# Kernel optimization log

Hardware: AMD Instinct MI355X
Metric: run time of the kernel (lower is better)

The kernel has to match this reference:

```python
import jax, jax.numpy as jnp
import numpy as np

LN_EPS = 1e-5


def _graph_conv(x, src, dst, W, b):
    # x: [N, D]; src, dst: [E]. Edge (src->dst): node n aggregates mean of
    # x[src] over edges whose dst == n (matches batch_edges[0][batch_edges[1]==n]).
    N = x.shape[0]
    agg_sum = jax.ops.segment_sum(x[src], dst, num_segments=N)            # [N, D]
    cnt = jax.ops.segment_sum(jnp.ones_like(src, dtype=x.dtype), dst, num_segments=N)
    agg = agg_sum / jnp.maximum(cnt, 1.0)[:, None]                        # zeros if no neighbors
    combined = jnp.concatenate([x, agg], axis=-1)                         # [N, 2D]
    return combined @ W + b


def _layer_norm(x, g, b):
    mu = jnp.mean(x, axis=-1, keepdims=True)
    var = jnp.var(x, axis=-1, keepdims=True)
    return (x - mu) * jax.lax.rsqrt(var + LN_EPS) * g + b


def setup_inputs() -> dict:
    key = jax.random.key(0)
    ks = jax.random.split(key, 16)
    B, N, E = 16, 10000, 160000
    IN, H, OUT, L = 19, 64, 32, 3
    s = lambda k, fan_in, shape: jax.random.normal(k, shape, jnp.float32) * (1.0 / np.sqrt(fan_in))
    return {
        "node_features": jax.random.normal(ks[0], (B, N, IN), jnp.float32),
        "edge_indices": jax.random.randint(ks[1], (B, 2, E), 0, N, jnp.int64),
        "batch_size": B,
        "enc_w1": s(ks[2], IN, (IN, H)), "enc_b1": jnp.zeros((H,), jnp.float32),
        "enc_w2": s(ks[3], H, (H, H)), "enc_b2": jnp.zeros((H,), jnp.float32),
        "conv_w": s(ks[4], 2 * H, (L, 2 * H, H)), "conv_b": jnp.zeros((L, H), jnp.float32),
        "ln_g": jnp.ones((L, H), jnp.float32), "ln_b": jnp.zeros((L, H), jnp.float32),
        "out_w": s(ks[5], H, (H, OUT)), "out_b": jnp.zeros((OUT,), jnp.float32),
    }


def reference(node_features, edge_indices, batch_size, enc_w1, enc_b1, enc_w2, enc_b2,
              conv_w, conv_b, ln_g, ln_b, out_w, out_b):
    # node encoder: Linear -> ReLU -> Linear
    x = jax.nn.relu(node_features @ enc_w1 + enc_b1) @ enc_w2 + enc_b2    # [B, N, H]
    src = edge_indices[:, 0, :]
    dst = edge_indices[:, 1, :]
    num_layers = conv_w.shape[0]
    conv = jax.vmap(_graph_conv, in_axes=(0, 0, 0, None, None))
    for i in range(num_layers):
        residual = x
        x = conv(x, src, dst, conv_w[i], conv_b[i])
        x = _layer_norm(x + residual, ln_g[i], ln_b[i])
        x = jax.nn.relu(x)
    return x @ out_w + out_b                                              # [B, N, 32]
```

## Files before the change

kernel.cpp:

```cpp
#include <hip/hip_runtime.h>
#include <hip/hip_fp16.h>

#define NB   16
#define NN   10000
#define NE   160000
#define NODES (NB*NN)
#define IN_F 19
#define HF   64
#define OUTF 32
#define LN_EPS 1e-5f
#define RANGE 625
#define NCHUNK 32
#define CHSZ (NE/NCHUNK)
#define BCAP 16384


__device__ inline unsigned pk_f16(float a, float b) {
    __half2 h = __float22half2_rn(float2{a, b});
    return *(unsigned*)&h;
}
__device__ inline float2 upk_f16(unsigned u) {
    __half2 h = *(__half2*)&u;
    return __half22float2(h);
}

__global__ __launch_bounds__(256) void enc1_kernel(
    const float* __restrict__ nf,
    const float* __restrict__ w1, const float* __restrict__ b1,
    __half* __restrict__ xh)
{
    int node = blockIdx.x * 256 + threadIdx.x;
    const float* p = nf + (size_t)node * IN_F;
    float a[IN_F];
#pragma unroll
    for (int k = 0; k < IN_F; ++k) a[k] = p[k];

    float h[HF];
#pragma unroll
    for (int j = 0; j < HF; ++j) h[j] = b1[j];
#pragma unroll
    for (int k = 0; k < IN_F; ++k) {
        float ak = a[k];
        const float* wr = w1 + k * HF;
#pragma unroll
        for (int j = 0; j < HF; ++j) h[j] = fmaf(ak, wr[j], h[j]);
    }

    uint4* dst = (uint4*)(xh + (size_t)node * HF);
#pragma unroll
    for (int q = 0; q < 8; ++q) {
        uint4 u;
        u.x = pk_f16(fmaxf(h[8*q+0],0.f), fmaxf(h[8*q+1],0.f));
        u.y = pk_f16(fmaxf(h[8*q+2],0.f), fmaxf(h[8*q+3],0.f));
        u.z = pk_f16(fmaxf(h[8*q+4],0.f), fmaxf(h[8*q+5],0.f));
        u.w = pk_f16(fmaxf(h[8*q+6],0.f), fmaxf(h[8*q+7],0.f));
        dst[q] = u;
    }
}

__global__ __launch_bounds__(256) void gemm64_kernel(
    __half* __restrict__ xh, const float* __restrict__ W, const float* __restrict__ bias)
{
    int lane = threadIdx.x & 63;
    int waveid = threadIdx.x >> 6;
    int half = __builtin_amdgcn_readfirstlane(waveid & 1);
    int nib = (waveid >> 1) * 64 + lane;
    int node = blockIdx.x * 128 + nib;
    const uint4* rp = (const uint4*)(xh + (size_t)node * HF);

    float acc[32];
    const float* b2 = bias + half * 32;
#pragma unroll
    for (int j = 0; j < 32; ++j) acc[j] = b2[j];

#pragma unroll 1
    for (int kc = 0; kc < HF; kc += 16) {
        uint4 u0 = rp[kc >> 3];
        uint4 u1 = rp[(kc >> 3) + 1];
        float av[16];
        float2 f;
        f = upk_f16(u0.x); av[0]=f.x;  av[1]=f.y;
        f = upk_f16(u0.y); av[2]=f.x;  av[3]=f.y;
        f = upk_f16(u0.z); av[4]=f.x;  av[5]=f.y;
        f = upk_f16(u0.w); av[6]=f.x;  av[7]=f.y;
        f = upk_f16(u1.x); av[8]=f.x;  av[9]=f.y;
        f = upk_f16(u1.y); av[10]=f.x; av[11]=f.y;
        f = upk_f16(u1.z); av[12]=f.x; av[13]=f.y;
        f = upk_f16(u1.w); av[14]=f.x; av[15]=f.y;
#pragma unroll
        for (int u = 0; u < 16; ++u) {
            const float* wr = W + (kc + u) * HF + half * 32;
#pragma unroll
            for (int j = 0; j < 32; ++j) acc[j] = fmaf(av[u], wr[j], acc[j]);
        }
    }

    __syncthreads();

    uint4* hdst = (uint4*)(xh + (size_t)node * HF + half * 32);
#pragma unroll
    for (int q = 0; q < 4; ++q) {
        uint4 u;
        u.x = pk_f16(acc[8*q+0], acc[8*q+1]);
        u.y = pk_f16(acc[8*q+2], acc[8*q+3]);
        u.z = pk_f16(acc[8*q+4], acc[8*q+5]);
        u.w = pk_f16(acc[8*q+6], acc[8*q+7]);
        hdst[q] = u;
    }
}

__global__ __launch_bounds__(256) void bucket_kernel(const int* __restrict__ ei,
                                                     int* __restrict__ gcur,
                                                     unsigned* __restrict__ bkt)
{
    __shared__ int lcnt[16];
    __shared__ int lcur[16];
    __shared__ int gbase[16];
    int b = blockIdx.x >> 5;
    int chunk = blockIdx.x & 31;
    int t = threadIdx.x;
    if (t < 16) { lcnt[t] = 0; lcur[t] = 0; }
    __syncthreads();

    const int* srcp = ei + (size_t)b * 2 * NE + chunk * CHSZ;
    const int* dstp = srcp + NE;

    for (int e = t; e < CHSZ; e += 256)
        atomicAdd(&lcnt[(unsigned)dstp[e] / RANGE], 1);
    __syncthreads();
    if (t < 16) gbase[t] = atomicAdd(&gcur[b * 16 + t], lcnt[t]);
    __syncthreads();

    for (int e = t; e < CHSZ; e += 256) {
        int d = dstp[e];
        int s = srcp[e];
        int j = (unsigned)d / RANGE;
        int ld = d - j * RANGE;
        int pos = gbase[j] + atomicAdd(&lcur[j], 1);
        if (pos < BCAP)
            bkt[(size_t)(b * 16 + j) * BCAP + pos] = (unsigned)s | ((unsigned)ld << 16);
    }
}

__global__ __launch_bounds__(512) void count2_kernel(const unsigned* __restrict__ bkt,
                                                     const int* __restrict__ gcur,
                                                     int* __restrict__ cnt)
{
    __shared__ int lcnt[RANGE];
    int bid = blockIdx.x;
    int b = bid >> 4, j = bid & 15;
    int t = threadIdx.x;
    for (int i = t; i < RANGE; i += 512) lcnt[i] = 0;
    __syncthreads();
    int n = min(gcur[bid], BCAP);
    const unsigned* bp = bkt + (size_t)bid * BCAP;
    for (int e = t; e < n; e += 512) atomicAdd(&lcnt[bp[e] >> 16], 1);
    __syncthreads();
    int base = b * NN + j * RANGE;
    for (int i = t; i < RANGE; i += 512) cnt[base + i] = lcnt[i];
}

__global__ __launch_bounds__(256) void scan_kernel(const int* __restrict__ cnt, int* __restrict__ off)
{
    __shared__ int sdata[256];
    int b = blockIdx.x, t = threadIdx.x;
    const int CH = 40;
    int lo = t * CH, hi = min(lo + CH, NN);
    int s = 0;
    for (int i = lo; i < hi; ++i) s += cnt[b * NN + i];
    sdata[t] = s;
    __syncthreads();
    for (int ofs = 1; ofs < 256; ofs <<= 1) {
        int v = (t >= ofs) ? sdata[t - ofs] : 0;
        __syncthreads();
        sdata[t] += v;
        __syncthreads();
    }
    int run = (t > 0) ? sdata[t - 1] : 0;
    for (int i = lo; i < hi; ++i) { off[b * NN + i] = run; run += cnt[b * NN + i]; }
}

__global__ __launch_bounds__(512) void fill2_kernel(const unsigned* __restrict__ bkt,
                                                    const int* __restrict__ gcur,
                                                    const int* __restrict__ off,
                                                    int* __restrict__ csr)
{
    __shared__ int lcur[RANGE];
    int bid = blockIdx.x;
    int b = bid >> 4, j = bid & 15;
    int t = threadIdx.x;
    for (int i = t; i < RANGE; i += 512) lcur[i] = 0;
    __syncthreads();
    int n = min(gcur[bid], BCAP);
    const unsigned* bp = bkt + (size_t)bid * BCAP;
    const int* offb = off + b * NN + j * RANGE;
    int* csrb = csr + (size_t)b * NE;
    for (int e = t; e < n; e += 512) {
        unsigned u = bp[e];
        int ld = u >> 16;
        int pos = offb[ld] + atomicAdd(&lcur[ld], 1);
        csrb[pos] = (int)(u & 0xffffu);
    }
}

__global__ __launch_bounds__(256) void agg_kernel(const __half* __restrict__ xh,
                                                  const int* __restrict__ cnt,
                                                  const int* __restrict__ off,
                                                  const int* __restrict__ csr,
                                                  __half* __restrict__ aggh)
{
    int b = blockIdx.x & 15;
    int chunk = blockIdx.x >> 4;
    int wid = threadIdx.x >> 6;
    int n = chunk * 4 + wid;
    int w = b * NN + n;
    w = __builtin_amdgcn_readfirstlane(w);
    int lane = threadIdx.x & 63;
    int g  = lane >> 5;
    int cl = lane & 31;
    int c = cnt[w];
    int o = off[w];
    const int* row = csr + (size_t)b * NE + o;
    const unsigned* xbu = (const unsigned*)(xh + (size_t)b * NN * HF);
    float a0 = 0.f, a1 = 0.f;
    int t = 0;
    for (; t + 8 <= c; t += 8) {
        int i0 = row[t],   i1 = row[t+1], i2 = row[t+2], i3 = row[t+3];
        int i4 = row[t+4], i5 = row[t+5], i6 = row[t+6], i7 = row[t+7];
        int j0 = g ? i1 : i0;
        int j1 = g ? i3 : i2;
        int j2 = g ? i5 : i4;
        int j3 = g ? i7 : i6;
        unsigned u0 = xbu[(size_t)j0 * 32 + cl];
        unsigned u1 = xbu[(size_t)j1 * 32 + cl];
        unsigned u2 = xbu[(size_t)j2 * 32 + cl];
        unsigned u3 = xbu[(size_t)j3 * 32 + cl];
        float2 f0 = upk_f16(u0), f1 = upk_f16(u1), f2 = upk_f16(u2), f3 = upk_f16(u3);
        a0 += f0.x; a1 += f0.y;
        a0 += f1.x; a1 += f1.y;
        a0 += f2.x; a1 += f2.y;
        a0 += f3.x; a1 += f3.y;
    }
    for (; t + 2 <= c; t += 2) {
        int i0 = row[t], i1 = row[t+1];
        int j = g ? i1 : i0;
        float2 f = upk_f16(xbu[(size_t)j * 32 + cl]);
        a0 += f.x; a1 += f.y;
    }
    if (t < c && g == 0) {
        float2 f = upk_f16(xbu[(size_t)row[t] * 32 + cl]);
        a0 += f.x; a1 += f.y;
    }
    a0 += __shfl_xor(a0, 32, 64);
    a1 += __shfl_xor(a1, 32, 64);
    float inv = (c > 0) ? 1.f / (float)c : 0.f;
    unsigned pk = pk_f16(a0 * inv, a1 * inv);
    if (g == 0) ((unsigned*)aggh)[(size_t)w * 32 + cl] = pk;
}

__global__ __launch_bounds__(256) void conv_kernel(
    __half* __restrict__ xh, const __half* __restrict__ aggh,
    const float* __restrict__ W, const float* __restrict__ bias,
    const float* __restrict__ g, const float* __restrict__ beta)
{
    __shared__ float s1[2][128];
    __shared__ float s2[2][128];
    int lane = threadIdx.x & 63;
    int waveid = threadIdx.x >> 6;
    int half = __builtin_amdgcn_readfirstlane(waveid & 1);
    int nib = (waveid >> 1) * 64 + lane;
    int node = blockIdx.x * 128 + nib;
    const uint4* xp = (const uint4*)(xh   + (size_t)node * HF);
    const uint4* ap = (const uint4*)(aggh + (size_t)node * HF);

    float acc[32];
    const float* b2 = bias + half * 32;
#pragma unroll
    for (int j = 0; j < 32; ++j) acc[j] = b2[j];

#pragma unroll 1
    for (int kc = 0; kc < HF; kc += 16) {
        uint4 u0 = ap[kc >> 3];
        uint4 u1 = ap[(kc >> 3) + 1];
        float av[16];
        float2 f;
        f = upk_f16(u0.x); av[0]=f.x;  av[1]=f.y;
        f = upk_f16(u0.y); av[2]=f.x;  av[3]=f.y;
        f = upk_f16(u0.z); av[4]=f.x;  av[5]=f.y;
        f = upk_f16(u0.w); av[6]=f.x;  av[7]=f.y;
        f = upk_f16(u1.x); av[8]=f.x;  av[9]=f.y;
        f = upk_f16(u1.y); av[10]=f.x; av[11]=f.y;
        f = upk_f16(u1.z); av[12]=f.x; av[13]=f.y;
        f = upk_f16(u1.w); av[14]=f.x; av[15]=f.y;
#pragma unroll
        for (int uu = 0; uu < 16; ++uu) {
            const float* wr = W + (HF + kc + uu) * HF + half * 32;
#pragma unroll
            for (int j = 0; j < 32; ++j) acc[j] = fmaf(av[uu], wr[j], acc[j]);
        }
    }

#pragma unroll 1
    for (int kc = 0; kc < HF; kc += 16) {
        uint4 u0 = xp[kc >> 3];
        uint4 u1 = xp[(kc >> 3) + 1];
        float av[16];
        float2 f;
        f = upk_f16(u0.x); av[0]=f.x;  av[1]=f.y;
        f = upk_f16(u0.y); av[2]=f.x;  av[3]=f.y;
        f = upk_f16(u0.z); av[4]=f.x;  av[5]=f.y;
        f = upk_f16(u0.w); av[6]=f.x;  av[7]=f.y;
        f = upk_f16(u1.x); av[8]=f.x;  av[9]=f.y;
        f = upk_f16(u1.y); av[10]=f.x; av[11]=f.y;
        f = upk_f16(u1.z); av[12]=f.x; av[13]=f.y;
        f = upk_f16(u1.w); av[14]=f.x; av[15]=f.y;
#pragma unroll
        for (int uu = 0; uu < 16; ++uu) {
            const float* wr = W + (kc + uu) * HF + half * 32;
#pragma unroll
            for (int j = 0; j < 32; ++j) acc[j] = fmaf(av[uu], wr[j], acc[j]);
        }
    }

    const uint4* xr = (const uint4*)(xh + (size_t)node * HF + half * 32);
#pragma unroll
    for (int q = 0; q < 4; ++q) {
        uint4 u = xr[q];
        float2 f;
        f = upk_f16(u.x); acc[8*q+0] += f.x; acc[8*q+1] += f.y;
        f = upk_f16(u.y); acc[8*q+2] += f.x; acc[8*q+3] += f.y;
        f = upk_f16(u.z); acc[8*q+4] += f.x; acc[8*q+5] += f.y;
        f = upk_f16(u.w); acc[8*q+6] += f.x; acc[8*q+7] += f.y;
    }
    float ps = 0.f, pq = 0.f;
#pragma unroll
    for (int j = 0; j < 32; ++j) { ps += acc[j]; pq += acc[j] * acc[j]; }
    s1[half][nib] = ps;
    s2[half][nib] = pq;
    __syncthreads();
    float sum = s1[0][nib] + s1[1][nib];
    float sq  = s2[0][nib] + s2[1][nib];
    float mu = sum * (1.f / HF);
    float var = sq * (1.f / HF) - mu * mu;
    float rs = rsqrtf(var + LN_EPS);

    const float* g2 = g + half * 32;
    const float* be2 = beta + half * 32;
#pragma unroll
    for (int j = 0; j < 32; ++j) {
        float y = (acc[j] - mu) * rs * g2[j] + be2[j];
        acc[j] = fmaxf(y, 0.f);
    }

    uint4* hdst = (uint4*)(xh + (size_t)node * HF + half * 32);
#pragma unroll
    for (int q = 0; q < 4; ++q) {
        uint4 u;
        u.x = pk_f16(acc[8*q+0], acc[8*q+1]);
        u.y = pk_f16(acc[8*q+2], acc[8*q+3]);
        u.z = pk_f16(acc[8*q+4], acc[8*q+5]);
        u.w = pk_f16(acc[8*q+6], acc[8*q+7]);
        hdst[q] = u;
    }
}

__global__ __launch_bounds__(256) void out_kernel(const __half* __restrict__ xh,
                                                  const float* __restrict__ W,
                                                  const float* __restrict__ bias,
                                                  float* __restrict__ out)
{
    int lane = threadIdx.x & 63;
    int waveid = threadIdx.x >> 6;
    int half = __builtin_amdgcn_readfirstlane(waveid & 1);
    int nib = (waveid >> 1) * 64 + lane;
    int node = blockIdx.x * 128 + nib;
    const uint4* rp = (const uint4*)(xh + (size_t)node * HF);

    float o[16];
    const float* b2 = bias + half * 16;
#pragma unroll
    for (int j = 0; j < 16; ++j) o[j] = b2[j];

#pragma unroll 1
    for (int kc = 0; kc < HF; kc += 16) {
        uint4 u0 = rp[kc >> 3];
        uint4 u1 = rp[(kc >> 3) + 1];
        float av[16];
        float2 f;
        f = upk_f16(u0.x); av[0]=f.x;  av[1]=f.y;
        f = upk_f16(u0.y); av[2]=f.x;  av[3]=f.y;
        f = upk_f16(u0.z); av[4]=f.x;  av[5]=f.y;
        f = upk_f16(u0.w); av[6]=f.x;  av[7]=f.y;
        f = upk_f16(u1.x); av[8]=f.x;  av[9]=f.y;
        f = upk_f16(u1.y); av[10]=f.x; av[11]=f.y;
        f = upk_f16(u1.z); av[12]=f.x; av[13]=f.y;
        f = upk_f16(u1.w); av[14]=f.x; av[15]=f.y;
#pragma unroll
        for (int u = 0; u < 16; ++u) {
            const float* wr = W + (kc + u) * OUTF + half * 16;
#pragma unroll
            for (int j = 0; j < 16; ++j) o[j] = fmaf(av[u], wr[j], o[j]);
        }
    }

    float4* dst = (float4*)(out + (size_t)node * OUTF + half * 16);
#pragma unroll
    for (int q = 0; q < 4; ++q) {
        float4 v; v.x = o[4*q]; v.y = o[4*q+1]; v.z = o[4*q+2]; v.w = o[4*q+3];
        dst[q] = v;
    }
}

extern "C" void kernel_launch(void* const* d_in, const int* in_sizes, int n_in,
                              void* d_out, int out_size, void* d_ws, size_t ws_size,
                              hipStream_t stream)
{
    const float* nf     = (const float*)d_in[0];
    const int*   ei     = (const int*)  d_in[1];
    const float* enc_w1 = (const float*)d_in[3];
    const float* enc_b1 = (const float*)d_in[4];
    const float* enc_w2 = (const float*)d_in[5];
    const float* enc_b2 = (const float*)d_in[6];
    const float* conv_w = (const float*)d_in[7];
    const float* conv_b = (const float*)d_in[8];
    const float* ln_g   = (const float*)d_in[9];
    const float* ln_b   = (const float*)d_in[10];
    const float* out_w  = (const float*)d_in[11];
    const float* out_b  = (const float*)d_in[12];

    char* w = (char*)d_ws;
    __half* xh   = (__half*)w;  w += (size_t)NODES * HF * 2;
    __half* agh  = (__half*)w;  w += (size_t)NODES * HF * 2;
    unsigned* bkt = (unsigned*)agh;
    int* cnt     = (int*)w;     w += (size_t)NODES * sizeof(int);
    int* off     = (int*)w;     w += (size_t)NODES * sizeof(int);
    int* csr     = (int*)w;     w += (size_t)NB * NE * sizeof(int);
    int* gcur    = (int*)w;

    hipMemsetAsync(gcur, 0, 256 * sizeof(int), stream);

    enc1_kernel<<<NODES / 256, 256, 0, stream>>>(nf, enc_w1, enc_b1, xh);
    gemm64_kernel<<<NODES / 128, 256, 0, stream>>>(xh, enc_w2, enc_b2);
    bucket_kernel<<<NB * NCHUNK, 256, 0, stream>>>(ei, gcur, bkt);
    count2_kernel<<<NB * 16, 512, 0, stream>>>(bkt, gcur, cnt);
    scan_kernel<<<NB, 256, 0, stream>>>(cnt, off);
    fill2_kernel<<<NB * 16, 512, 0, stream>>>(bkt, gcur, off, csr);

    for (int l = 0; l < 3; ++l) {
        agg_kernel<<<NODES / 4, 256, 0, stream>>>(xh, cnt, off, csr, agh);
        conv_kernel<<<NODES / 128, 256, 0, stream>>>(xh, agh,
                                                     conv_w + (size_t)l * 2 * HF * HF,
                                                     conv_b + (size_t)l * HF,
                                                     ln_g + (size_t)l * HF,
                                                     ln_b + (size_t)l * HF);
    }
    out_kernel<<<NODES / 128, 256, 0, stream>>>(xh, out_w, out_b, (float*)d_out);
}
```

Baseline: 456.1 us.

## Use MFMA f16 matrix instructions for graph conv GEMM with LDS-staged weights

Rewrites the conv kernel to stage the 128x64 weight matrix in LDS as transposed fp16, then compute each 16-node tile with 16x16x32 f16 MFMA instructions instead of scalar FP32 FMAs. Results go through a shared buffer and are redistributed so four threads per node apply bias, residual, layernorm (via shuffles) and ReLU. This cuts ALU work in the per-layer dense transform. In exchange it rounds the weights to fp16 and adds a per-block weight staging step and an extra barrier.

```diff
diff --git a/kernel.cpp b/kernel.cpp
--- a/kernel.cpp
+++ b/kernel.cpp
@@ -23,6 +23,9 @@
     __half2 h = *(__half2*)&u;
     return __half22float2(h);
 }
+
+typedef _Float16 f16x8 __attribute__((ext_vector_type(8)));
+typedef float    f32x4 __attribute__((ext_vector_type(4)));
 
 __global__ __launch_bounds__(256) void enc1_kernel(
     const float* __restrict__ nf,
@@ -263,105 +266,100 @@
     const float* __restrict__ W, const float* __restrict__ bias,
     const float* __restrict__ g, const float* __restrict__ beta)
 {
-    __shared__ float s1[2][128];
-    __shared__ float s2[2][128];
-    int lane = threadIdx.x & 63;
-    int waveid = threadIdx.x >> 6;
-    int half = __builtin_amdgcn_readfirstlane(waveid & 1);
-    int nib = (waveid >> 1) * 64 + lane;
-    int node = blockIdx.x * 128 + nib;
-    const uint4* xp = (const uint4*)(xh   + (size_t)node * HF);
-    const uint4* ap = (const uint4*)(aggh + (size_t)node * HF);
-
-    float acc[32];
-    const float* b2 = bias + half * 32;
-#pragma unroll
-    for (int j = 0; j < 32; ++j) acc[j] = b2[j];
-
-#pragma unroll 1
-    for (int kc = 0; kc < HF; kc += 16) {
-        uint4 u0 = ap[kc >> 3];
-        uint4 u1 = ap[(kc >> 3) + 1];
-        float av[16];
+    __shared__ __half Wt[64][136];
+    __shared__ float s_out[64][68];
+
+    int t = threadIdx.x;
+
+    {
+        int c  = t & 63;
+        int kb = (t >> 6) * 32;
+#pragma unroll
+        for (int k = 0; k < 32; k += 2) {
+            float w0 = W[(size_t)(kb + k)     * HF + c];
+            float w1 = W[(size_t)(kb + k + 1) * HF + c];
+            *(__half2*)&Wt[c][kb + k] = __float22half2_rn(float2{w0, w1});
+        }
+    }
+    __syncthreads();
+
+    int l     = t & 63;
+    int wv    = t >> 6;
+    int arow16 = l & 15;
+    int ks    = (l >> 4) * 8;
+    int node  = blockIdx.x * 64 + wv * 16 + arow16;
+
+    const __half* xrow = xh   + (size_t)node * HF;
+    const __half* grow = aggh + (size_t)node * HF;
+    f16x8 a0 = *(const f16x8*)(xrow + ks);
+    f16x8 a1 = *(const f16x8*)(xrow + 32 + ks);
+    f16x8 a2 = *(const f16x8*)(grow + ks);
+    f16x8 a3 = *(const f16x8*)(grow + 32 + ks);
+
+    int orow = wv * 16 + (l >> 4) * 4;
+#pragma unroll
+    for (int ct = 0; ct < 4; ++ct) {
+        int col = (l & 15) + ct * 16;
+        f16x8 b0 = *(const f16x8*)&Wt[col][ks];
+        f16x8 b1 = *(const f16x8*)&Wt[col][32 + ks];
+        f16x8 b2 = *(const f16x8*)&Wt[col][64 + ks];
+        f16x8 b3 = *(const f16x8*)&Wt[col][96 + ks];
+        f32x4 acc = {0.f, 0.f, 0.f, 0.f};
+        acc = __builtin_amdgcn_mfma_f32_16x16x32_f16(a0, b0, acc, 0, 0, 0);
+        acc = __builtin_amdgcn_mfma_f32_16x16x32_f16(a1, b1, acc, 0, 0, 0);
+        acc = __builtin_amdgcn_mfma_f32_16x16x32_f16(a2, b2, acc, 0, 0, 0);
+        acc = __builtin_amdgcn_mfma_f32_16x16x32_f16(a3, b3, acc, 0, 0, 0);
+#pragma unroll
+        for (int j = 0; j < 4; ++j)
+            s_out[orow + j][col] = acc[j];
+    }
+    __syncthreads();
+
+    int nb = t >> 2;
+    int q  = t & 3;
+    int node2 = blockIdx.x * 64 + nb;
+    const float* srow = &s_out[nb][q * 16];
+    const float* b2   = bias + q * 16;
+    float v[16];
+#pragma unroll
+    for (int i = 0; i < 16; ++i) v[i] = srow[i] + b2[i];
+
+    const uint4* xr = (const uint4*)(xh + (size_t)node2 * HF + q * 16);
+    uint4 r0 = xr[0], r1 = xr[1];
+    {
         float2 f;
-        f = upk_f16(u0.x); av[0]=f.x;  av[1]=f.y;
-        f = upk_f16(u0.y); av[2]=f.x;  av[3]=f.y;
-        f = upk_f16(u0.z); av[4]=f.x;  av[5]=f.y;
-        f = upk_f16(u0.w); av[6]=f.x;  av[7]=f.y;
-        f = upk_f16(u1.x); av[8]=f.x;  av[9]=f.y;
-        f = upk_f16(u1.y); av[10]=f.x; av[11]=f.y;
-        f = upk_f16(u1.z); av[12]=f.x; av[13]=f.y;
-        f = upk_f16(u1.w); av[14]=f.x; av[15]=f.y;
-#pragma unroll
-        for (int uu = 0; uu < 16; ++uu) {
-            const float* wr = W + (HF + kc + uu) * HF + half * 32;
-#pragma unroll
-            for (int j = 0; j < 32; ++j) acc[j] = fmaf(av[uu], wr[j], acc[j]);
-        }
-    }
-
-#pragma unroll 1
-    for (int kc = 0; kc < HF; kc += 16) {
-        uint4 u0 = xp[kc >> 3];
-        uint4 u1 = xp[(kc >> 3) + 1];
-        float av[16];
-        float2 f;
-        f = upk_f16(u0.x); av[0]=f.x;  av[1]=f.y;
-        f = upk_f16(u0.y); av[2]=f.x;  av[3]=f.y;
-        f = upk_f16(u0.z); av[4]=f.x;  av[5]=f.y;
-        f = upk_f16(u0.w); av[6]=f.x;  av[7]=f.y;
-        f = upk_f16(u1.x); av[8]=f.x;  av[9]=f.y;
-        f = upk_f16(u1.y); av[10]=f.x; av[11]=f.y;
-        f = upk_f16(u1.z); av[12]=f.x; av[13]=f.y;
-        f = upk_f16(u1.w); av[14]=f.x; av[15]=f.y;
-#pragma unroll
-        for (int uu = 0; uu < 16; ++uu) {
-            const float* wr = W + (kc + uu) * HF + half * 32;
-#pragma unroll
-            for (int j = 0; j < 32; ++j) acc[j] = fmaf(av[uu], wr[j], acc[j]);
-        }
-    }
-
-    const uint4* xr = (const uint4*)(xh + (size_t)node * HF + half * 32);
-#pragma unroll
-    for (int q = 0; q < 4; ++q) {
-        uint4 u = xr[q];
-        float2 f;
-        f = upk_f16(u.x); acc[8*q+0] += f.x; acc[8*q+1] += f.y;
-        f = upk_f16(u.y); acc[8*q+2] += f.x; acc[8*q+3] += f.y;
-        f = upk_f16(u.z); acc[8*q+4] += f.x; acc[8*q+5] += f.y;
-        f = upk_f16(u.w); acc[8*q+6] += f.x; acc[8*q+7] += f.y;
+        f = upk_f16(r0.x); v[0] += f.x;  v[1] += f.y;
+        f = upk_f16(r0.y); v[2] += f.x;  v[3] += f.y;
+        f = upk_f16(r0.z); v[4] += f.x;  v[5] += f.y;
+        f = upk_f16(r0.w); v[6] += f.x;  v[7] += f.y;
+        f = upk_f16(r1.x); v[8] += f.x;  v[9] += f.y;
+        f = upk_f16(r1.y); v[10] += f.x; v[11] += f.y;
+        f = upk_f16(r1.z); v[12] += f.x; v[13] += f.y;
+        f = upk_f16(r1.w); v[14] += f.x; v[15] += f.y;
     }
     float ps = 0.f, pq = 0.f;
 #pragma unroll
-    for (int j = 0; j < 32; ++j) { ps += acc[j]; pq += acc[j] * acc[j]; }
-    s1[half][nib] = ps;
-    s2[half][nib] = pq;
-    __syncthreads();
-    float sum = s1[0][nib] + s1[1][nib];
-    float sq  = s2[0][nib] + s2[1][nib];
-    float mu = sum * (1.f / HF);
-    float var = sq * (1.f / HF) - mu * mu;
-    float rs = rsqrtf(var + LN_EPS);
-
-    const float* g2 = g + half * 32;
-    const float* be2 = beta + half * 32;
-#pragma unroll
-    for (int j = 0; j < 32; ++j) {
-        float y = (acc[j] - mu) * rs * g2[j] + be2[j];
-        acc[j] = fmaxf(y, 0.f);
-    }
-
-    uint4* hdst = (uint4*)(xh + (size_t)node * HF + half * 32);
-#pragma unroll
-    for (int q = 0; q < 4; ++q) {
-        uint4 u;
-        u.x = pk_f16(acc[8*q+0], acc[8*q+1]);
-        u.y = pk_f16(acc[8*q+2], acc[8*q+3]);
-        u.z = pk_f16(acc[8*q+4], acc[8*q+5]);
-        u.w = pk_f16(acc[8*q+6], acc[8*q+7]);
-        hdst[q] = u;
-    }
+    for (int i = 0; i < 16; ++i) { ps += v[i]; pq += v[i] * v[i]; }
+    ps += __shfl_xor(ps, 1, 64); ps += __shfl_xor(ps, 2, 64);
+    pq += __shfl_xor(pq, 1, 64); pq += __shfl_xor(pq, 2, 64);
+    float mu  = ps * (1.f / HF);
+    float var = pq * (1.f / HF) - mu * mu;
+    float rs  = rsqrtf(var + LN_EPS);
+
+    const float* g2  = g    + q * 16;
+    const float* be2 = beta + q * 16;
+    float y[16];
+#pragma unroll
+    for (int i = 0; i < 16; ++i)
+        y[i] = fmaxf((v[i] - mu) * rs * g2[i] + be2[i], 0.f);
+
+    uint4* hdst = (uint4*)(xh + (size_t)node2 * HF + q * 16);
+    uint4 o0, o1;
+    o0.x = pk_f16(y[0],  y[1]);  o0.y = pk_f16(y[2],  y[3]);
+    o0.z = pk_f16(y[4],  y[5]);  o0.w = pk_f16(y[6],  y[7]);
+    o1.x = pk_f16(y[8],  y[9]);  o1.y = pk_f16(y[10], y[11]);
+    o1.z = pk_f16(y[12], y[13]); o1.w = pk_f16(y[14], y[15]);
+    hdst[0] = o0; hdst[1] = o1;
 }
 
 __global__ __launch_bounds__(256) void out_kernel(const __half* __restrict__ xh,
@@ -448,11 +446,11 @@
 
     for (int l = 0; l < 3; ++l) {
         agg_kernel<<<NODES / 4, 256, 0, stream>>>(xh, cnt, off, csr, agh);
-        conv_kernel<<<NODES / 128, 256, 0, stream>>>(xh, agh,
-                                                     conv_w + (size_t)l * 2 * HF * HF,
-                                                     conv_b + (size_t)l * HF,
-                                                     ln_g + (size_t)l * HF,
-                                                     ln_b + (size_t)l * HF);
+        conv_kernel<<<NODES / 64, 256, 0, stream>>>(xh, agh,
+                                                    conv_w + (size_t)l * 2 * HF * HF,
+                                                    conv_b + (size_t)l * HF,
+                                                    ln_g + (size_t)l * HF,
+                                                    ln_b + (size_t)l * HF);
     }
     out_kernel<<<NODES / 128, 256, 0, stream>>>(xh, out_w, out_b, (float*)d_out);
 }
```

Measured after the change: 404.6 us. -11.3%, faster.
